# Optimization experiments

Hardware: AMD Instinct MI355X
Metric: run time of the kernel (lower is better)

## Reference

```python
import jax, jax.numpy as jnp
import numpy as np

N = 10000      # nodes
E = 160000     # directed edges (avg degree 16)
F_IN = 2208    # num_features (DenseNet-161 dim)
H = 512        # hidden_channels
C = 2          # num_classes


def setup_inputs() -> dict:
    key = jax.random.key(0)
    ks = jax.random.split(key, 10)
    x = jax.random.normal(ks[0], (N, F_IN), dtype=jnp.float32)
    edge_index = jax.random.randint(ks[1], (2, E), 0, N, dtype=jnp.int64)
    batch = jnp.zeros((N,), dtype=jnp.int64)

    def glorot(k, fan_in, fan_out):
        s = np.sqrt(6.0 / (fan_in + fan_out)).astype(np.float32)
        return jax.random.uniform(k, (fan_in, fan_out), jnp.float32, -s, s)

    return {
        "x": x,
        "edge_index": edge_index,
        "batch": batch,
        "W1": glorot(ks[2], F_IN, H), "b1": jnp.zeros((H,), jnp.float32),
        "W2": glorot(ks[3], H, H),    "b2": jnp.zeros((H,), jnp.float32),
        "W3": glorot(ks[4], H, H),    "b3": jnp.zeros((H,), jnp.float32),
        "W4": glorot(ks[5], H, C),    "b4": jnp.zeros((C,), jnp.float32),
    }


def reference(x, edge_index, batch, W1, b1, W2, b2, W3, b3, W4, b4):
    # GCNConv (PyG defaults): add self-loops, symmetric normalization
    # out = D^{-1/2} (A + I) D^{-1/2} X W + b. Norm depends only on the
    # graph, so compute it once and reuse across the 4 layers.
    src, dst = edge_index[0], edge_index[1]
    loop = jnp.arange(N, dtype=edge_index.dtype)
    s = jnp.concatenate([src, loop])  # [E+N]
    d = jnp.concatenate([dst, loop])  # [E+N]
    deg = jax.ops.segment_sum(jnp.ones(E + N, x.dtype), d, num_segments=N)
    dinv = jnp.where(deg > 0, jax.lax.rsqrt(deg), 0.0)
    norm = dinv[s] * dinv[d]          # [E+N] per-edge weight

    def conv(h, W, b):
        h = h @ W                                 # [N, out] dense GEMM first (PyG order)
        msg = h[s] * norm[:, None]                # gather + scale  [E+N, out]
        return jax.ops.segment_sum(msg, d, num_segments=N) + b

    h = jax.nn.relu(conv(x, W1, b1))   # dropout p=0.3 is identity in eval mode
    h = jax.nn.relu(conv(h, W2, b2))
    h = jax.nn.relu(conv(h, W3, b3))
    h = conv(h, W4, b4)
    return jax.nn.log_softmax(h, axis=1)
```

## Files before the change

kernel.cpp:

```cpp
#include <hip/hip_runtime.h>
#include <hip/hip_bf16.h>

#define NNODES 10000
#define NEDGES 160000
#define FIN    2208
#define HDIM   512
#define NCLS   2

#define MPAD   10240
#define K1PAD  2240

typedef __bf16 bf16x8 __attribute__((ext_vector_type(8)));
typedef float  f32x4  __attribute__((ext_vector_type(4)));
typedef unsigned short u16x8 __attribute__((ext_vector_type(8)));

__device__ inline unsigned short f2bf(float f) {
    union { float f; unsigned int u; } v; v.f = f;
    return (unsigned short)((v.u + 0x7FFFu + ((v.u >> 16) & 1u)) >> 16);
}
__device__ inline float bf2f(unsigned short u) {
    union { unsigned int i; float f; } v; v.i = ((unsigned int)u) << 16; return v.f;
}


__global__ void k_init(int* cnt, int* row_cnt, int n) {
    int i = blockIdx.x * blockDim.x + threadIdx.x;
    if (i < n) { cnt[i] = 0; row_cnt[i] = 0; }
}

__global__ void k_hist(const int* __restrict__ ei, int* __restrict__ cnt, int e) {
    int i = blockIdx.x * blockDim.x + threadIdx.x;
    if (i < e) atomicAdd(&cnt[ei[NEDGES + i]], 1);
}

__global__ void k_scan(const int* __restrict__ cnt, int* __restrict__ row_ptr,
                       float* __restrict__ dinv, int n) {
    __shared__ int wsum[16];
    __shared__ int s_carry;
    int tid = threadIdx.x;
    int lane = tid & 63, wid = tid >> 6;
    if (tid == 0) { s_carry = 0; row_ptr[0] = 0; }
    __syncthreads();
    for (int base = 0; base < n; base += 1024) {
        int i = base + tid;
        int deg = (i < n) ? cnt[i] : 0;
        if (i < n) dinv[i] = rsqrtf((float)deg + 1.0f);
        int v = deg;
        #pragma unroll
        for (int off = 1; off < 64; off <<= 1) {
            int t = __shfl_up(v, off);
            if (lane >= off) v += t;
        }
        if (lane == 63) wsum[wid] = v;
        __syncthreads();
        if (wid == 0) {
            int s = (lane < 16) ? wsum[lane] : 0;
            #pragma unroll
            for (int off = 1; off < 16; off <<= 1) {
                int t = __shfl_up(s, off);
                if (lane >= off) s += t;
            }
            if (lane < 16) wsum[lane] = s;
        }
        __syncthreads();
        int add = s_carry + ((wid > 0) ? wsum[wid - 1] : 0);
        if (i < n) row_ptr[i + 1] = v + add;
        __syncthreads();
        if (tid == 1023) s_carry += wsum[15];
        __syncthreads();
    }
}

__global__ void k_fill(const int* __restrict__ ei, const int* __restrict__ row_ptr,
                       int* __restrict__ row_cnt, int* __restrict__ col_src, int e) {
    int i = blockIdx.x * blockDim.x + threadIdx.x;
    if (i < e) {
        int src = ei[i];
        int dst = ei[NEDGES + i];
        int pos = row_ptr[dst] + atomicAdd(&row_cnt[dst], 1);
        col_src[pos] = src;
    }
}


__global__ void k_cvt_x(const float* __restrict__ x, unsigned short* __restrict__ xb) {
    int row = blockIdx.x;
    int t = threadIdx.x;
    unsigned short* orow = xb + (size_t)row * K1PAD;
    u16x8 z = {0, 0, 0, 0, 0, 0, 0, 0};
    if (row >= NNODES) {
        for (int c = t; c < K1PAD / 8; c += 256) *(u16x8*)(orow + c * 8) = z;
        return;
    }
    const float* irow = x + (size_t)row * FIN;
    for (int c = t; c < K1PAD / 8; c += 256) {
        int col = c * 8;
        u16x8 o = z;
        if (col + 8 <= FIN) {
            float4 f0 = *(const float4*)(irow + col);
            float4 f1 = *(const float4*)(irow + col + 4);
            o[0] = f2bf(f0.x); o[1] = f2bf(f0.y); o[2] = f2bf(f0.z); o[3] = f2bf(f0.w);
            o[4] = f2bf(f1.x); o[5] = f2bf(f1.y); o[6] = f2bf(f1.z); o[7] = f2bf(f1.w);
        }
        *(u16x8*)(orow + col) = o;
    }
}

__global__ void k_cvt_w(const float* __restrict__ W1, const float* __restrict__ W2,
                        const float* __restrict__ W3, unsigned short* __restrict__ W1t,
                        unsigned short* __restrict__ W2t, unsigned short* __restrict__ W3t) {
    int n = blockIdx.y;
    int bx = blockIdx.x;
    int t = threadIdx.x;
    if (bx < 9) {
        int k = bx * 256 + t;
        if (k < K1PAD) {
            float v = (k < FIN) ? W1[(size_t)k * HDIM + n] : 0.0f;
            W1t[(size_t)n * K1PAD + k] = f2bf(v);
        }
    } else if (bx < 11) {
        int k = (bx - 9) * 256 + t;
        W2t[(size_t)n * HDIM + k] = f2bf(W2[(size_t)k * HDIM + n]);
    } else {
        int k = (bx - 11) * 256 + t;
        W3t[(size_t)n * HDIM + k] = f2bf(W3[(size_t)k * HDIM + n]);
    }
}


#define BKK 64

__global__ __launch_bounds__(256) void k_gemm_bf16(
    const unsigned short* __restrict__ A,
    const unsigned short* __restrict__ Bt,
    unsigned short* __restrict__ C,
    int M, int K) {
    __shared__ char As[128 * BKK * 2] __attribute__((aligned(16)));
    __shared__ char Bs[64 * BKK * 2]  __attribute__((aligned(16)));
    const int tid  = threadIdx.x;
    const int lane = tid & 63;
    const int w    = tid >> 6;
    const int wm   = w & 1, wn = w >> 1;
    const int quad = lane >> 4, lq = lane & 15;

    const int l     = blockIdx.x;
    const int xcd   = l & 7;
    const int q     = l >> 3;
    const int strip = (q >> 3) * 8 + xcd;
    const int bm    = strip * 128;
    const int bn    = (q & 7) * 64;

    f32x4 acc[4][2] = {};

    for (int k0 = 0; k0 < K; k0 += BKK) {
        #pragma unroll
        for (int i = 0; i < 4; ++i) {
            int c  = i * 256 + tid;
            int r  = c >> 3;
            int g  = (c & 7) ^ (r & 7);
            const char* gpA = (const char*)A + ((size_t)(bm + r) * K + k0) * 2 + (g << 4);
            __builtin_amdgcn_global_load_lds(
                (const __attribute__((address_space(1))) void*)gpA,
                (__attribute__((address_space(3))) void*)(As + c * 16), 16, 0, 0);
        }
        #pragma unroll
        for (int i = 0; i < 2; ++i) {
            int c  = i * 256 + tid;
            int r  = c >> 3;
            int g  = (c & 7) ^ (r & 7);
            const char* gpB = (const char*)Bt + ((size_t)(bn + r) * K + k0) * 2 + (g << 4);
            __builtin_amdgcn_global_load_lds(
                (const __attribute__((address_space(1))) void*)gpB,
                (__attribute__((address_space(3))) void*)(Bs + c * 16), 16, 0, 0);
        }
        __syncthreads();

        #pragma unroll
        for (int s = 0; s < 2; ++s) {
            bf16x8 af[4], bfr[2];
            int g = s * 4 + quad;
            #pragma unroll
            for (int i = 0; i < 4; ++i) {
                int r = wm * 64 + i * 16 + lq;
                af[i] = *(const bf16x8*)(As + r * 128 + ((g ^ (r & 7)) << 4));
            }
            #pragma unroll
            for (int j = 0; j < 2; ++j) {
                int n = wn * 32 + j * 16 + lq;
                bfr[j] = *(const bf16x8*)(Bs + n * 128 + ((g ^ (n & 7)) << 4));
            }
            #pragma unroll
            for (int i = 0; i < 4; ++i)
                #pragma unroll
                for (int j = 0; j < 2; ++j)
                    acc[i][j] = __builtin_amdgcn_mfma_f32_16x16x32_bf16(
                        af[i], bfr[j], acc[i][j], 0, 0, 0);
        }
        __syncthreads();
    }

    #pragma unroll
    for (int i = 0; i < 4; ++i) {
        #pragma unroll
        for (int p = 0; p < 4; ++p) {
            int r = bm + wm * 64 + i * 16 + quad * 4 + p;
            if (r < M) {
                #pragma unroll
                for (int j = 0; j < 2; ++j) {
                    int col = bn + wn * 32 + j * 16 + lq;
                    C[(size_t)r * HDIM + col] = f2bf(acc[i][j][p]);
                }
            }
        }
    }
}


__global__ void k_agg(const unsigned short* __restrict__ Y, const float* __restrict__ dinv,
                      const int* __restrict__ row_ptr, const int* __restrict__ col_src,
                      const float* __restrict__ bias, unsigned short* __restrict__ Hb,
                      int do_relu) {
    int w = (blockIdx.x * blockDim.x + threadIdx.x) >> 6;
    int lane = threadIdx.x & 63;
    if (w >= MPAD) return;
    unsigned short* hr = Hb + (size_t)w * HDIM + lane * 8;
    if (w >= NNODES) {
        u16x8 z = {0, 0, 0, 0, 0, 0, 0, 0};
        *(u16x8*)hr = z;
        return;
    }
    float di = dinv[w];
    float sw = di * di;
    u16x8 own = *(const u16x8*)(Y + (size_t)w * HDIM + lane * 8);
    float acc[8];
    #pragma unroll
    for (int t = 0; t < 8; ++t) acc[t] = sw * bf2f(own[t]);

    int e0 = row_ptr[w], e1 = row_ptr[w + 1];
    int e = e0;
    for (; e + 4 <= e1; e += 4) {
        int s0 = col_src[e + 0], s1 = col_src[e + 1];
        int s2 = col_src[e + 2], s3 = col_src[e + 3];
        float w0 = di * dinv[s0], w1 = di * dinv[s1];
        float w2 = di * dinv[s2], w3 = di * dinv[s3];
        u16x8 v0 = *(const u16x8*)(Y + (size_t)s0 * HDIM + lane * 8);
        u16x8 v1 = *(const u16x8*)(Y + (size_t)s1 * HDIM + lane * 8);
        u16x8 v2 = *(const u16x8*)(Y + (size_t)s2 * HDIM + lane * 8);
        u16x8 v3 = *(const u16x8*)(Y + (size_t)s3 * HDIM + lane * 8);
        #pragma unroll
        for (int t = 0; t < 8; ++t) {
            acc[t] += w0 * bf2f(v0[t]);
            acc[t] += w1 * bf2f(v1[t]);
            acc[t] += w2 * bf2f(v2[t]);
            acc[t] += w3 * bf2f(v3[t]);
        }
    }
    for (; e < e1; ++e) {
        int s = col_src[e];
        float wg = di * dinv[s];
        u16x8 v = *(const u16x8*)(Y + (size_t)s * HDIM + lane * 8);
        #pragma unroll
        for (int t = 0; t < 8; ++t) acc[t] += wg * bf2f(v[t]);
    }

    float4 b0 = ((const float4*)bias)[lane * 2];
    float4 b1 = ((const float4*)bias)[lane * 2 + 1];
    acc[0] += b0.x; acc[1] += b0.y; acc[2] += b0.z; acc[3] += b0.w;
    acc[4] += b1.x; acc[5] += b1.y; acc[6] += b1.z; acc[7] += b1.w;
    u16x8 o;
    #pragma unroll
    for (int t = 0; t < 8; ++t) {
        float v = acc[t];
        if (do_relu) v = fmaxf(v, 0.0f);
        o[t] = f2bf(v);
    }
    *(u16x8*)hr = o;
}


__global__ void k_gemm4(const unsigned short* __restrict__ H, const float* __restrict__ W4,
                        float* __restrict__ Y4, int n) {
    int w = (blockIdx.x * blockDim.x + threadIdx.x) >> 6;
    int lane = threadIdx.x & 63;
    if (w >= n) return;
    const unsigned short* hr = H + (size_t)w * HDIM + lane * 8;
    ushort4 hA = *(const ushort4*)hr;
    ushort4 hB = *(const ushort4*)(hr + 4);
    float hv[8] = {bf2f(hA.x), bf2f(hA.y), bf2f(hA.z), bf2f(hA.w),
                   bf2f(hB.x), bf2f(hB.y), bf2f(hB.z), bf2f(hB.w)};
    const float4* wf = (const float4*)W4;
    float4 w0 = wf[lane * 4 + 0];
    float4 w1 = wf[lane * 4 + 1];
    float4 w2 = wf[lane * 4 + 2];
    float4 w3 = wf[lane * 4 + 3];
    float acc0 = hv[0]*w0.x + hv[1]*w0.z + hv[2]*w1.x + hv[3]*w1.z
               + hv[4]*w2.x + hv[5]*w2.z + hv[6]*w3.x + hv[7]*w3.z;
    float acc1 = hv[0]*w0.y + hv[1]*w0.w + hv[2]*w1.y + hv[3]*w1.w
               + hv[4]*w2.y + hv[5]*w2.w + hv[6]*w3.y + hv[7]*w3.w;
    #pragma unroll
    for (int off = 32; off > 0; off >>= 1) {
        acc0 += __shfl_down(acc0, off);
        acc1 += __shfl_down(acc1, off);
    }
    if (lane == 0) {
        Y4[2 * w] = acc0;
        Y4[2 * w + 1] = acc1;
    }
}


__global__ void k_final(const float* __restrict__ Y4, const float* __restrict__ dinv,
                        const int* __restrict__ row_ptr, const int* __restrict__ col_src,
                        const float* __restrict__ b4, float* __restrict__ out, int n) {
    int i = blockIdx.x * blockDim.x + threadIdx.x;
    if (i >= n) return;
    float di = dinv[i];
    float sw = di * di;
    float z0 = sw * Y4[2 * i];
    float z1 = sw * Y4[2 * i + 1];
    int e0 = row_ptr[i], e1 = row_ptr[i + 1];
    for (int e = e0; e < e1; ++e) {
        int s = col_src[e];
        float wgt = di * dinv[s];
        z0 += wgt * Y4[2 * s];
        z1 += wgt * Y4[2 * s + 1];
    }
    z0 += b4[0];
    z1 += b4[1];
    float m = fmaxf(z0, z1);
    float l = m + logf(expf(z0 - m) + expf(z1 - m));
    out[2 * i] = z0 - l;
    out[2 * i + 1] = z1 - l;
}


extern "C" void kernel_launch(void* const* d_in, const int* in_sizes, int n_in,
                              void* d_out, int out_size, void* d_ws, size_t ws_size,
                              hipStream_t stream) {
    const float* x  = (const float*)d_in[0];
    const int*   ei = (const int*)d_in[1];
    const float* W1 = (const float*)d_in[3];
    const float* b1 = (const float*)d_in[4];
    const float* W2 = (const float*)d_in[5];
    const float* b2 = (const float*)d_in[6];
    const float* W3 = (const float*)d_in[7];
    const float* b3 = (const float*)d_in[8];
    const float* W4 = (const float*)d_in[9];
    const float* b4 = (const float*)d_in[10];
    float* out = (float*)d_out;

    char* ws = (char*)d_ws;
    float*          dinv    = (float*)(ws + 0);
    int*            cnt     = (int*)  (ws + 40960);
    int*            row_cnt = (int*)  (ws + 81920);
    int*            row_ptr = (int*)  (ws + 122880);
    int*            col_src = (int*)  (ws + 163840);
    float*          Y4      = (float*)(ws + 803840);
    unsigned short* xb      = (unsigned short*)(ws + 884224);
    unsigned short* W1t     = (unsigned short*)(ws + 46759424);
    unsigned short* W2t     = (unsigned short*)(ws + 49053184);
    unsigned short* W3t     = (unsigned short*)(ws + 49577472);
    unsigned short* Yb      = (unsigned short*)(ws + 50101760);
    unsigned short* Hb      = (unsigned short*)(ws + 60587520);
    if (ws_size < 71073280) return;

    k_init<<<40, 256, 0, stream>>>(cnt, row_cnt, NNODES);
    k_hist<<<625, 256, 0, stream>>>(ei, cnt, NEDGES);
    k_scan<<<1, 1024, 0, stream>>>(cnt, row_ptr, dinv, NNODES);
    k_fill<<<625, 256, 0, stream>>>(ei, row_ptr, row_cnt, col_src, NEDGES);

    k_cvt_x<<<MPAD, 256, 0, stream>>>(x, xb);
    k_cvt_w<<<dim3(13, HDIM), 256, 0, stream>>>(W1, W2, W3, W1t, W2t, W3t);

    const int ggrid = (MPAD / 128) * 8;
    const int agrid = (MPAD * 64) / 256;

    k_gemm_bf16<<<ggrid, 256, 0, stream>>>(xb, W1t, Yb, NNODES, K1PAD);
    k_agg<<<agrid, 256, 0, stream>>>(Yb, dinv, row_ptr, col_src, b1, Hb, 1);
    k_gemm_bf16<<<ggrid, 256, 0, stream>>>(Hb, W2t, Yb, NNODES, HDIM);
    k_agg<<<agrid, 256, 0, stream>>>(Yb, dinv, row_ptr, col_src, b2, Hb, 1);
    k_gemm_bf16<<<ggrid, 256, 0, stream>>>(Hb, W3t, Yb, NNODES, HDIM);
    k_agg<<<agrid, 256, 0, stream>>>(Yb, dinv, row_ptr, col_src, b3, Hb, 1);
    k_gemm4<<<2500, 256, 0, stream>>>(Hb, W4, Y4, NNODES);
    k_final<<<40, 256, 0, stream>>>(Y4, dinv, row_ptr, col_src, b4, out, NNODES);
}
```

Baseline: 346.0 us.

## Fuse x fp32-to-bf16 conversion into first GEMM and fuse layer-3 aggregation with W4

The first GEMM now reads fp32 x directly, converting to bf16 in registers before writing to LDS, which removes the separate conversion pass and its 45 MB round trip. The third aggregation is fused with the 512x2 projection, so Hb is no longer written and re-read. The counter-zeroing kernel is also merged into the weight-transpose kernel to save a launch. In exchange, the first GEMM now uses synchronous register loads of fp32 A (twice the bytes per tile) instead of async global-to-LDS copies, so memory latency is less hidden in the largest GEMM.

```diff
diff --git a/kernel.cpp b/kernel.cpp
--- a/kernel.cpp
+++ b/kernel.cpp
@@ -21,11 +21,34 @@
 __device__ inline float bf2f(unsigned short u) {
     union { unsigned int i; float f; } v; v.i = ((unsigned int)u) << 16; return v.f;
 }
-
-
-__global__ void k_init(int* cnt, int* row_cnt, int n) {
-    int i = blockIdx.x * blockDim.x + threadIdx.x;
-    if (i < n) { cnt[i] = 0; row_cnt[i] = 0; }
+__device__ inline unsigned int pack2bf(float a, float b) {
+    union { float f; unsigned int u; } ua, ub; ua.f = a; ub.f = b;
+    return ((ub.u + 0x8000u) & 0xFFFF0000u) | ((ua.u + 0x8000u) >> 16);
+}
+
+__global__ void k_prep(const float* __restrict__ W1, const float* __restrict__ W2,
+                       const float* __restrict__ W3, unsigned short* __restrict__ W1t,
+                       unsigned short* __restrict__ W2t, unsigned short* __restrict__ W3t,
+                       int* __restrict__ cnt, int* __restrict__ row_cnt) {
+    int n = blockIdx.y;
+    int bx = blockIdx.x;
+    int t = threadIdx.x;
+    if (bx < 9) {
+        int k = bx * 256 + t;
+        if (k < K1PAD) {
+            float v = (k < FIN) ? W1[(size_t)k * HDIM + n] : 0.0f;
+            W1t[(size_t)n * K1PAD + k] = f2bf(v);
+        }
+    } else if (bx < 11) {
+        int k = (bx - 9) * 256 + t;
+        W2t[(size_t)n * HDIM + k] = f2bf(W2[(size_t)k * HDIM + n]);
+    } else if (bx < 13) {
+        int k = (bx - 11) * 256 + t;
+        W3t[(size_t)n * HDIM + k] = f2bf(W3[(size_t)k * HDIM + n]);
+    } else {
+        int i = n * 256 + t;
+        if (i < NNODES) { cnt[i] = 0; row_cnt[i] = 0; }
+    }
 }
 
 __global__ void k_hist(const int* __restrict__ ei, int* __restrict__ cnt, int e) {
@@ -83,52 +106,102 @@
 }
 
 
-__global__ void k_cvt_x(const float* __restrict__ x, unsigned short* __restrict__ xb) {
-    int row = blockIdx.x;
-    int t = threadIdx.x;
-    unsigned short* orow = xb + (size_t)row * K1PAD;
-    u16x8 z = {0, 0, 0, 0, 0, 0, 0, 0};
-    if (row >= NNODES) {
-        for (int c = t; c < K1PAD / 8; c += 256) *(u16x8*)(orow + c * 8) = z;
-        return;
-    }
-    const float* irow = x + (size_t)row * FIN;
-    for (int c = t; c < K1PAD / 8; c += 256) {
-        int col = c * 8;
-        u16x8 o = z;
-        if (col + 8 <= FIN) {
-            float4 f0 = *(const float4*)(irow + col);
-            float4 f1 = *(const float4*)(irow + col + 4);
-            o[0] = f2bf(f0.x); o[1] = f2bf(f0.y); o[2] = f2bf(f0.z); o[3] = f2bf(f0.w);
-            o[4] = f2bf(f1.x); o[5] = f2bf(f1.y); o[6] = f2bf(f1.z); o[7] = f2bf(f1.w);
-        }
-        *(u16x8*)(orow + col) = o;
-    }
-}
-
-__global__ void k_cvt_w(const float* __restrict__ W1, const float* __restrict__ W2,
-                        const float* __restrict__ W3, unsigned short* __restrict__ W1t,
-                        unsigned short* __restrict__ W2t, unsigned short* __restrict__ W3t) {
-    int n = blockIdx.y;
-    int bx = blockIdx.x;
-    int t = threadIdx.x;
-    if (bx < 9) {
-        int k = bx * 256 + t;
-        if (k < K1PAD) {
-            float v = (k < FIN) ? W1[(size_t)k * HDIM + n] : 0.0f;
-            W1t[(size_t)n * K1PAD + k] = f2bf(v);
-        }
-    } else if (bx < 11) {
-        int k = (bx - 9) * 256 + t;
-        W2t[(size_t)n * HDIM + k] = f2bf(W2[(size_t)k * HDIM + n]);
-    } else {
-        int k = (bx - 11) * 256 + t;
-        W3t[(size_t)n * HDIM + k] = f2bf(W3[(size_t)k * HDIM + n]);
-    }
-}
-
-
 #define BKK 64
+
+__global__ __launch_bounds__(256) void k_gemm1(
+    const float* __restrict__ A,
+    const unsigned short* __restrict__ Bt,
+    unsigned short* __restrict__ C,
+    int M) {
+    __shared__ char As[128 * BKK * 2] __attribute__((aligned(16)));
+    __shared__ char Bs[64 * BKK * 2]  __attribute__((aligned(16)));
+    const int tid  = threadIdx.x;
+    const int lane = tid & 63;
+    const int w    = tid >> 6;
+    const int wm   = w & 1, wn = w >> 1;
+    const int quad = lane >> 4, lq = lane & 15;
+
+    const int l     = blockIdx.x;
+    const int xcd   = l & 7;
+    const int q     = l >> 3;
+    const int strip = (q >> 3) * 8 + xcd;
+    const int bm    = strip * 128;
+    const int bn    = (q & 7) * 64;
+
+    f32x4 acc[4][2] = {};
+
+    for (int k0 = 0; k0 < K1PAD; k0 += BKK) {
+        #pragma unroll
+        for (int i = 0; i < 4; ++i) {
+            int c = i * 256 + tid;
+            int r = c >> 3;
+            int g = (c & 7) ^ (r & 7);
+            int row = bm + r;
+            if (row >= NNODES) row = NNODES - 1;
+            int col = k0 + g * 8;
+            uint4 pk = {0u, 0u, 0u, 0u};
+            if (col < FIN) {
+                const float4* p = (const float4*)(A + (size_t)row * FIN + col);
+                float4 f0 = p[0], f1 = p[1];
+                pk.x = pack2bf(f0.x, f0.y);
+                pk.y = pack2bf(f0.z, f0.w);
+                pk.z = pack2bf(f1.x, f1.y);
+                pk.w = pack2bf(f1.z, f1.w);
+            }
+            *(uint4*)(As + c * 16) = pk;
+        }
+        #pragma unroll
+        for (int i = 0; i < 2; ++i) {
+            int c = i * 256 + tid;
+            int r = c >> 3;
+            int g = (c & 7) ^ (r & 7);
+            const char* gpB = (const char*)Bt + ((size_t)(bn + r) * K1PAD + k0) * 2 + (g << 4);
+            __builtin_amdgcn_global_load_lds(
+                (const __attribute__((address_space(1))) void*)gpB,
+                (__attribute__((address_space(3))) void*)(Bs + c * 16), 16, 0, 0);
+        }
+        __syncthreads();
+
+        #pragma unroll
+        for (int s = 0; s < 2; ++s) {
+            bf16x8 af[4], bfr[2];
+            int g = s * 4 + quad;
+            #pragma unroll
+            for (int i = 0; i < 4; ++i) {
+                int r = wm * 64 + i * 16 + lq;
+                af[i] = *(const bf16x8*)(As + r * 128 + ((g ^ (r & 7)) << 4));
+            }
+            #pragma unroll
+            for (int j = 0; j < 2; ++j) {
+                int n = wn * 32 + j * 16 + lq;
+                bfr[j] = *(const bf16x8*)(Bs + n * 128 + ((g ^ (n & 7)) << 4));
+            }
+            #pragma unroll
+            for (int i = 0; i < 4; ++i)
+                #pragma unroll
+                for (int j = 0; j < 2; ++j)
+                    acc[i][j] = __builtin_amdgcn_mfma_f32_16x16x32_bf16(
+                        af[i], bfr[j], acc[i][j], 0, 0, 0);
+        }
+        __syncthreads();
+    }
+
+    #pragma unroll
+    for (int i = 0; i < 4; ++i) {
+        #pragma unroll
+        for (int p = 0; p < 4; ++p) {
+            int r = bm + wm * 64 + i * 16 + quad * 4 + p;
+            if (r < M) {
+                #pragma unroll
+                for (int j = 0; j < 2; ++j) {
+                    int col = bn + wn * 32 + j * 16 + lq;
+                    C[(size_t)r * HDIM + col] = f2bf(acc[i][j][p]);
+                }
+            }
+        }
+    }
+}
+
 
 __global__ __launch_bounds__(256) void k_gemm_bf16(
     const unsigned short* __restrict__ A,
@@ -155,9 +228,9 @@
     for (int k0 = 0; k0 < K; k0 += BKK) {
         #pragma unroll
         for (int i = 0; i < 4; ++i) {
-            int c  = i * 256 + tid;
-            int r  = c >> 3;
-            int g  = (c & 7) ^ (r & 7);
+            int c = i * 256 + tid;
+            int r = c >> 3;
+            int g = (c & 7) ^ (r & 7);
             const char* gpA = (const char*)A + ((size_t)(bm + r) * K + k0) * 2 + (g << 4);
             __builtin_amdgcn_global_load_lds(
                 (const __attribute__((address_space(1))) void*)gpA,
@@ -165,9 +238,9 @@
         }
         #pragma unroll
         for (int i = 0; i < 2; ++i) {
-            int c  = i * 256 + tid;
-            int r  = c >> 3;
-            int g  = (c & 7) ^ (r & 7);
+            int c = i * 256 + tid;
+            int r = c >> 3;
+            int g = (c & 7) ^ (r & 7);
             const char* gpB = (const char*)Bt + ((size_t)(bn + r) * K + k0) * 2 + (g << 4);
             __builtin_amdgcn_global_load_lds(
                 (const __attribute__((address_space(1))) void*)gpB,
@@ -218,8 +291,7 @@
 
 __global__ void k_agg(const unsigned short* __restrict__ Y, const float* __restrict__ dinv,
                       const int* __restrict__ row_ptr, const int* __restrict__ col_src,
-                      const float* __restrict__ bias, unsigned short* __restrict__ Hb,
-                      int do_relu) {
+                      const float* __restrict__ bias, unsigned short* __restrict__ Hb) {
     int w = (blockIdx.x * blockDim.x + threadIdx.x) >> 6;
     int lane = threadIdx.x & 63;
     if (w >= MPAD) return;
@@ -269,42 +341,76 @@
     acc[4] += b1.x; acc[5] += b1.y; acc[6] += b1.z; acc[7] += b1.w;
     u16x8 o;
     #pragma unroll
-    for (int t = 0; t < 8; ++t) {
-        float v = acc[t];
-        if (do_relu) v = fmaxf(v, 0.0f);
-        o[t] = f2bf(v);
-    }
+    for (int t = 0; t < 8; ++t) o[t] = f2bf(fmaxf(acc[t], 0.0f));
     *(u16x8*)hr = o;
 }
 
 
-__global__ void k_gemm4(const unsigned short* __restrict__ H, const float* __restrict__ W4,
-                        float* __restrict__ Y4, int n) {
+__global__ void k_agg_g4(const unsigned short* __restrict__ Y, const float* __restrict__ dinv,
+                         const int* __restrict__ row_ptr, const int* __restrict__ col_src,
+                         const float* __restrict__ b3, const float* __restrict__ W4,
+                         float* __restrict__ Y4) {
     int w = (blockIdx.x * blockDim.x + threadIdx.x) >> 6;
     int lane = threadIdx.x & 63;
-    if (w >= n) return;
-    const unsigned short* hr = H + (size_t)w * HDIM + lane * 8;
-    ushort4 hA = *(const ushort4*)hr;
-    ushort4 hB = *(const ushort4*)(hr + 4);
-    float hv[8] = {bf2f(hA.x), bf2f(hA.y), bf2f(hA.z), bf2f(hA.w),
-                   bf2f(hB.x), bf2f(hB.y), bf2f(hB.z), bf2f(hB.w)};
+    if (w >= NNODES) return;
+    float di = dinv[w];
+    float sw = di * di;
+    u16x8 own = *(const u16x8*)(Y + (size_t)w * HDIM + lane * 8);
+    float acc[8];
+    #pragma unroll
+    for (int t = 0; t < 8; ++t) acc[t] = sw * bf2f(own[t]);
+
+    int e0 = row_ptr[w], e1 = row_ptr[w + 1];
+    int e = e0;
+    for (; e + 4 <= e1; e += 4) {
+        int s0 = col_src[e + 0], s1 = col_src[e + 1];
+        int s2 = col_src[e + 2], s3 = col_src[e + 3];
+        float w0 = di * dinv[s0], w1 = di * dinv[s1];
+        float w2 = di * dinv[s2], w3 = di * dinv[s3];
+        u16x8 v0 = *(const u16x8*)(Y + (size_t)s0 * HDIM + lane * 8);
+        u16x8 v1 = *(const u16x8*)(Y + (size_t)s1 * HDIM + lane * 8);
+        u16x8 v2 = *(const u16x8*)(Y + (size_t)s2 * HDIM + lane * 8);
+        u16x8 v3 = *(const u16x8*)(Y + (size_t)s3 * HDIM + lane * 8);
+        #pragma unroll
+        for (int t = 0; t < 8; ++t) {
+            acc[t] += w0 * bf2f(v0[t]);
+            acc[t] += w1 * bf2f(v1[t]);
+            acc[t] += w2 * bf2f(v2[t]);
+            acc[t] += w3 * bf2f(v3[t]);
+        }
+    }
+    for (; e < e1; ++e) {
+        int s = col_src[e];
+        float wg = di * dinv[s];
+        u16x8 v = *(const u16x8*)(Y + (size_t)s * HDIM + lane * 8);
+        #pragma unroll
+        for (int t = 0; t < 8; ++t) acc[t] += wg * bf2f(v[t]);
+    }
+
+    float4 b0 = ((const float4*)b3)[lane * 2];
+    float4 b1 = ((const float4*)b3)[lane * 2 + 1];
+    acc[0] += b0.x; acc[1] += b0.y; acc[2] += b0.z; acc[3] += b0.w;
+    acc[4] += b1.x; acc[5] += b1.y; acc[6] += b1.z; acc[7] += b1.w;
+    #pragma unroll
+    for (int t = 0; t < 8; ++t) acc[t] = fmaxf(acc[t], 0.0f);
+
     const float4* wf = (const float4*)W4;
     float4 w0 = wf[lane * 4 + 0];
     float4 w1 = wf[lane * 4 + 1];
     float4 w2 = wf[lane * 4 + 2];
     float4 w3 = wf[lane * 4 + 3];
-    float acc0 = hv[0]*w0.x + hv[1]*w0.z + hv[2]*w1.x + hv[3]*w1.z
-               + hv[4]*w2.x + hv[5]*w2.z + hv[6]*w3.x + hv[7]*w3.z;
-    float acc1 = hv[0]*w0.y + hv[1]*w0.w + hv[2]*w1.y + hv[3]*w1.w
-               + hv[4]*w2.y + hv[5]*w2.w + hv[6]*w3.y + hv[7]*w3.w;
+    float z0 = acc[0]*w0.x + acc[1]*w0.z + acc[2]*w1.x + acc[3]*w1.z
+             + acc[4]*w2.x + acc[5]*w2.z + acc[6]*w3.x + acc[7]*w3.z;
+    float z1 = acc[0]*w0.y + acc[1]*w0.w + acc[2]*w1.y + acc[3]*w1.w
+             + acc[4]*w2.y + acc[5]*w2.w + acc[6]*w3.y + acc[7]*w3.w;
     #pragma unroll
     for (int off = 32; off > 0; off >>= 1) {
-        acc0 += __shfl_down(acc0, off);
-        acc1 += __shfl_down(acc1, off);
+        z0 += __shfl_down(z0, off);
+        z1 += __shfl_down(z1, off);
     }
     if (lane == 0) {
-        Y4[2 * w] = acc0;
-        Y4[2 * w + 1] = acc1;
+        Y4[2 * w] = z0;
+        Y4[2 * w + 1] = z1;
     }
 }
 
@@ -356,31 +462,26 @@
     int*            row_ptr = (int*)  (ws + 122880);
     int*            col_src = (int*)  (ws + 163840);
     float*          Y4      = (float*)(ws + 803840);
-    unsigned short* xb      = (unsigned short*)(ws + 884224);
-    unsigned short* W1t     = (unsigned short*)(ws + 46759424);
-    unsigned short* W2t     = (unsigned short*)(ws + 49053184);
-    unsigned short* W3t     = (unsigned short*)(ws + 49577472);
-    unsigned short* Yb      = (unsigned short*)(ws + 50101760);
-    unsigned short* Hb      = (unsigned short*)(ws + 60587520);
-    if (ws_size < 71073280) return;
-
-    k_init<<<40, 256, 0, stream>>>(cnt, row_cnt, NNODES);
+    unsigned short* W1t     = (unsigned short*)(ws + 884224);
+    unsigned short* W2t     = (unsigned short*)(ws + 3177984);
+    unsigned short* W3t     = (unsigned short*)(ws + 3702272);
+    unsigned short* Yb      = (unsigned short*)(ws + 4226560);
+    unsigned short* Hb      = (unsigned short*)(ws + 14712320);
+    if (ws_size < 25198080) return;
+
+    k_prep<<<dim3(14, HDIM), 256, 0, stream>>>(W1, W2, W3, W1t, W2t, W3t, cnt, row_cnt);
     k_hist<<<625, 256, 0, stream>>>(ei, cnt, NEDGES);
     k_scan<<<1, 1024, 0, stream>>>(cnt, row_ptr, dinv, NNODES);
     k_fill<<<625, 256, 0, stream>>>(ei, row_ptr, row_cnt, col_src, NEDGES);
 
-    k_cvt_x<<<MPAD, 256, 0, stream>>>(x, xb);
-    k_cvt_w<<<dim3(13, HDIM), 256, 0, stream>>>(W1, W2, W3, W1t, W2t, W3t);
-
     const int ggrid = (MPAD / 128) * 8;
     const int agrid = (MPAD * 64) / 256;
 
-    k_gemm_bf16<<<ggrid, 256, 0, stream>>>(xb, W1t, Yb, NNODES, K1PAD);
-    k_agg<<<agrid, 256, 0, stream>>>(Yb, dinv, row_ptr, col_src, b1, Hb, 1);
+    k_gemm1<<<ggrid, 256, 0, stream>>>(x, W1t, Yb, NNODES);
+    k_agg<<<agrid, 256, 0, stream>>>(Yb, dinv, row_ptr, col_src, b1, Hb);
     k_gemm_bf16<<<ggrid, 256, 0, stream>>>(Hb, W2t, Yb, NNODES, HDIM);
-    k_agg<<<agrid, 256, 0, stream>>>(Yb, dinv, row_ptr, col_src, b2, Hb, 1);
+    k_agg<<<agrid, 256, 0, stream>>>(Yb, dinv, row_ptr, col_src, b2, Hb);
     k_gemm_bf16<<<ggrid, 256, 0, stream>>>(Hb, W3t, Yb, NNODES, HDIM);
-    k_agg<<<agrid, 256, 0, stream>>>(Yb, dinv, row_ptr, col_src, b3, Hb, 1);
-    k_gemm4<<<2500, 256, 0, stream>>>(Hb, W4, Y4, NNODES);
+    k_agg_g4<<<(NNODES * 64) / 256, 256, 0, stream>>>(Yb, dinv, row_ptr, col_src, b3, W4, Y4);
     k_final<<<40, 256, 0, stream>>>(Y4, dinv, row_ptr, col_src, b4, out, NNODES);
 }
```

New measurement: 393.1 us. 13.6% more time.
